# Kernel tuning notes

Measured on AMD Instinct MI355X. Metric: run time of the kernel, lower is better.

Reference implementation:

```python
import jax, jax.numpy as jnp
import numpy as np

HEAD = 8
D_Q = 64
NEG_INF = -1e9
EPS = 1e-9


def setup_inputs() -> dict:
    key = jax.random.key(0)
    ks = jax.random.split(key, 5)
    bs, seq_len, d_model = 4, 1024, 512
    context = jax.random.normal(ks[0], (bs, seq_len, d_model), dtype=jnp.float32)
    attention_mask = jnp.ones((bs, seq_len), dtype=jnp.int32)
    # nn.Linear default init: U(-1/sqrt(fan_in), 1/sqrt(fan_in))
    bound = 1.0 / np.sqrt(d_model)
    Wq = jax.random.uniform(ks[1], (HEAD * D_Q, d_model), jnp.float32, -bound, bound)
    bq = jax.random.uniform(ks[2], (HEAD * D_Q,), jnp.float32, -bound, bound)
    Wk = jax.random.uniform(ks[3], (HEAD * D_Q, d_model), jnp.float32, -bound, bound)
    bk = jax.random.uniform(ks[4], (HEAD * D_Q,), jnp.float32, -bound, bound)
    return {"context": context, "attention_mask": attention_mask,
            "Wq": Wq, "bq": bq, "Wk": Wk, "bk": bk}


def reference(context, attention_mask, Wq, bq, Wk, bk):
    bs, seq_len, d_model = context.shape
    # structural masks
    after_mask = jnp.eye(seq_len, k=1, dtype=jnp.int32)    # superdiagonal
    prev_mask = jnp.eye(seq_len, k=-1, dtype=jnp.int32)    # subdiagonal
    self_mask = jnp.eye(seq_len, dtype=jnp.int32)          # diagonal
    summing_op = jnp.triu(jnp.ones((seq_len, seq_len), jnp.float32))  # upper-tri ones

    # attention_mask & (after + prev): (bs,1,1,S) & (S,S) -> (bs,1,S,S)
    mask = attention_mask[:, None, None, :] & (after_mask + prev_mask)

    # projections -> (bs, head, seq, d_q)
    q = (context @ Wq.T + bq).reshape(bs, seq_len, HEAD, D_Q).transpose(0, 2, 1, 3)
    k = (context @ Wk.T + bk).reshape(bs, seq_len, HEAD, D_Q).transpose(0, 2, 1, 3)

    scores = jnp.einsum('bhqd,bhkd->bhqk', q, k) / d_model
    scores = jnp.where(mask == 0, NEG_INF, scores)
    scores = jax.nn.softmax(scores, axis=-1)

    # geometric-mean fusion of forward/backward neighbor scores
    phrasal_attn = jnp.sqrt(scores * jnp.swapaxes(scores, -2, -1) + EPS)
    # prior_attn = 0 (default): phrasal_attn = 0 + (1-0)*phrasal_attn

    # log-cumsum via triangular matmuls
    p = jnp.where(after_mask == 0, 0.0, jnp.log(phrasal_attn + EPS))  # (bs,h,S,S)
    p = jnp.einsum('bhij,jk->bhik', p, summing_op)
    attn = jnp.exp(jnp.einsum('ij,bhjk->bhik', summing_op, p))
    # zero out on-and-below diagonal (keep strict upper triangle)
    strict_upper = summing_op.astype(jnp.int32) - self_mask
    attn = jnp.where(strict_upper == 0, 0.0, attn)
    attn = attn + jnp.swapaxes(attn, -2, -1) + jnp.where(self_mask == 0, EPS, phrasal_attn)
    return (attn, phrasal_attn)
```

## Files before the change

kernel.cpp:

```cpp
#include <hip/hip_runtime.h>
#include <hip/hip_bf16.h>

#define BS 4
#define SEQ 1024
#define DM 512
#define NQK 1024
#define NROW (BS*SEQ)
#define EPS 1e-9f
#define SQRTEPS 3.16227766e-5f

typedef __attribute__((ext_vector_type(8))) short short8;
typedef __attribute__((ext_vector_type(4))) float floatx4;

__global__ __launch_bounds__(256) void convert_kernel(
    const float* __restrict__ ctx, const float* __restrict__ Wq,
    const float* __restrict__ Wk, unsigned short* __restrict__ Xbf,
    unsigned short* __restrict__ Wbf)
{
    int idx = blockIdx.x * 256 + threadIdx.x;
    {
        unsigned int u = __float_as_uint(ctx[idx]);
        Xbf[idx] = (unsigned short)((u + 0x7fffu + ((u >> 16) & 1u)) >> 16);
    }
    if (idx < DM * DM) {
        unsigned int a = __float_as_uint(Wq[idx]);
        Wbf[idx] = (unsigned short)((a + 0x7fffu + ((a >> 16) & 1u)) >> 16);
        unsigned int c = __float_as_uint(Wk[idx]);
        Wbf[DM * DM + idx] = (unsigned short)((c + 0x7fffu + ((c >> 16) & 1u)) >> 16);
    }
}

#define BM 64
#define BN 64
#define BK 32
#define LDA 40
#define NGEMM 1024
#define NBG   4096

__global__ __launch_bounds__(256) void gemm_qk_bg(
    const unsigned short* __restrict__ X, const unsigned short* __restrict__ W,
    const float* __restrict__ bq, const float* __restrict__ bk,
    float* __restrict__ QK, float* __restrict__ phrasal)
{
    __shared__ unsigned short As[BM * LDA];
    __shared__ unsigned short Bs[BN * LDA];

    const int id  = blockIdx.x;
    const int tid = threadIdx.x;

    if (id >= NGEMM) {
        const int bb = id - NGEMM;
        float* base = phrasal + (size_t)bb * 8192;
        floatx4 v4 = {SQRTEPS, SQRTEPS, SQRTEPS, SQRTEPS};
        #pragma unroll
        for (int j = 0; j < 8; ++j)
            *(floatx4*)(base + (size_t)(j * 256 + tid) * 4) = v4;
        return;
    }

    const int bm   = id & 63;
    const int bn   = id >> 6;
    const int wave = tid >> 6;
    const int lane = tid & 63;
    const int wm   = wave >> 1, wn = wave & 1;
    const int lr   = lane & 15;
    const int kg   = lane >> 4;

    const int srow = tid >> 2;
    const int skc  = (tid & 3) << 3;
    const unsigned short* Xp = X + (size_t)(bm * BM + srow) * DM + skc;
    const unsigned short* Wp = W + (size_t)(bn * BN + srow) * DM + skc;

    floatx4 acc[2][2] = {};

    for (int k0 = 0; k0 < DM; k0 += BK) {
        uint4 va = *(const uint4*)(Xp + k0);
        uint4 vb = *(const uint4*)(Wp + k0);
        __syncthreads();
        *(uint4*)(As + srow * LDA + skc) = va;
        *(uint4*)(Bs + srow * LDA + skc) = vb;
        __syncthreads();

        short8 a[2], b[2];
        #pragma unroll
        for (int mi = 0; mi < 2; ++mi)
            a[mi] = *(const short8*)(As + (wm * 32 + mi * 16 + lr) * LDA + kg * 8);
        #pragma unroll
        for (int ni = 0; ni < 2; ++ni)
            b[ni] = *(const short8*)(Bs + (wn * 32 + ni * 16 + lr) * LDA + kg * 8);
        #pragma unroll
        for (int mi = 0; mi < 2; ++mi)
            #pragma unroll
            for (int ni = 0; ni < 2; ++ni)
                acc[mi][ni] = __builtin_amdgcn_mfma_f32_16x16x32_bf16(
                    a[mi], b[ni], acc[mi][ni], 0, 0, 0);
    }

    #pragma unroll
    for (int mi = 0; mi < 2; ++mi) {
        #pragma unroll
        for (int ni = 0; ni < 2; ++ni) {
            int n = bn * BN + wn * 32 + ni * 16 + lr;
            float bias = (n < DM) ? bq[n] : bk[n - DM];
            #pragma unroll
            for (int r = 0; r < 4; ++r) {
                int m = bm * BM + wm * 32 + mi * 16 + kg * 4 + r;
                QK[(size_t)m * NQK + n] = acc[mi][ni][r] + bias;
            }
        }
    }
}

__global__ __launch_bounds__(256) void dot_kernel(
    const float* __restrict__ QK, float* __restrict__ uArr, float* __restrict__ vArr)
{
    const int gw   = blockIdx.x * 4 + (threadIdx.x >> 6);
    const int lane = threadIdx.x & 63;
    const int bh   = gw >> 10;
    const int i    = gw & 1023;
    const int b    = bh >> 3, h = bh & 7;

    float u = 0.f, v = 0.f;
    if (i < SEQ - 1) {
        const float* r0 = QK + (size_t)(b * SEQ + i)     * NQK;
        const float* r1 = QK + (size_t)(b * SEQ + i + 1) * NQK;
        float qi  = r0[h * 64 + lane];
        float ki  = r0[DM + h * 64 + lane];
        float qi1 = r1[h * 64 + lane];
        float ki1 = r1[DM + h * 64 + lane];
        float pu = qi * ki1, pv = qi1 * ki;
        #pragma unroll
        for (int m = 1; m < 64; m <<= 1) {
            pu += __shfl_xor(pu, m);
            pv += __shfl_xor(pv, m);
        }
        u = pu * (1.0f / DM);
        v = pv * (1.0f / DM);
    }
    if (lane == 0) { uArr[gw] = u; vArr[gw] = v; }
}

__global__ __launch_bounds__(1024) void gscan_kernel(
    const float* __restrict__ uArr, const float* __restrict__ vArr,
    const int* __restrict__ am, float* __restrict__ gArr, float* __restrict__ CArr)
{
    __shared__ double wsum[16];

    const int bh   = blockIdx.x;
    const int b    = bh >> 3;
    const int i    = threadIdx.x;
    const int base = bh * SEQ;

    float g = 0.f;
    if (i < SEQ - 1) {
        float u   = uArr[base + i];
        float vv  = vArr[base + i];
        int   im1 = (i > 0) ? i - 1 : 0;
        float vm1 = vArr[base + im1];
        float up1 = uArr[base + i + 1];
        int mL = (i > 0) ? am[b * SEQ + i - 1] : 0;
        int mR = am[b * SEQ + i + 1];
        float s_up = mR ? (mL ? 1.f / (1.f + expf(vm1 - u)) : 1.f) : 0.f;
        int mL2 = am[b * SEQ + i];
        int mR2 = (i + 2 < SEQ) ? am[b * SEQ + i + 2] : 0;
        float s_dn = mL2 ? (mR2 ? 1.f / (1.f + expf(up1 - vv)) : 1.f) : 0.f;
        g = sqrtf(s_up * s_dn + EPS);
        gArr[base + i] = g;
    }

    double L = (i < SEQ - 1) ? (double)logf(g + EPS) : 0.0;
    double x = L;
    const int lane = i & 63, wv = i >> 6;
    #pragma unroll
    for (int off = 1; off < 64; off <<= 1) {
        double t = __shfl_up(x, off);
        if (lane >= off) x += t;
    }
    if (lane == 63) wsum[wv] = x;
    __syncthreads();
    double pref = 0.0;
    for (int w = 0; w < wv; ++w) pref += wsum[w];
    CArr[base + i] = (float)(pref + x - L);
}

__global__ __launch_bounds__(256) void fill_attn(
    const float* __restrict__ gArr, const float* __restrict__ CArr,
    float* __restrict__ attn, float* __restrict__ phrasal)
{
    const int row = blockIdx.x;
    const int bh  = row >> 10;
    const int i   = row & 1023;
    const int t   = threadIdx.x;

    const float Ci = CArr[row];
    floatx4 c4 = *(const floatx4*)(CArr + bh * SEQ + t * 4);
    floatx4 av;
    #pragma unroll
    for (int j = 0; j < 4; ++j) {
        int k = t * 4 + j;
        float d = (k > i) ? (c4[j] - Ci) : (Ci - c4[j]);
        av[j] = (k == i) ? SQRTEPS : (__expf(d) + EPS);
    }
    *(floatx4*)(attn + (size_t)row * SEQ + t * 4) = av;

    if (t == 0) {
        if (i > 0)
            phrasal[(size_t)row * SEQ + i - 1] = gArr[bh * SEQ + i - 1];
        if (i < SEQ - 1)
            phrasal[(size_t)row * SEQ + i + 1] = gArr[bh * SEQ + i];
    }
}

extern "C" void kernel_launch(void* const* d_in, const int* in_sizes, int n_in,
                              void* d_out, int out_size, void* d_ws, size_t ws_size,
                              hipStream_t stream) {
    const float* ctx = (const float*)d_in[0];
    const int*   am  = (const int*)d_in[1];
    const float* Wq  = (const float*)d_in[2];
    const float* bq  = (const float*)d_in[3];
    const float* Wk  = (const float*)d_in[4];
    const float* bk  = (const float*)d_in[5];
    float* out = (float*)d_out;

    char* ws = (char*)d_ws;
    unsigned short* Xbf = (unsigned short*)(ws);
    unsigned short* Wbf = (unsigned short*)(ws + 4194304);
    float*          QK  = (float*)(ws + 5242880);
    float*          uA  = (float*)(ws + 22020096);
    float*          vA  = (float*)(ws + 22151168);
    float*          gA  = (float*)(ws + 22282240);
    float*          CA  = (float*)(ws + 22413312);

    float* attn_out    = out;
    float* phrasal_out = out + (size_t)BS * 8 * SEQ * SEQ;

    convert_kernel<<<dim3(BS * SEQ * DM / 256), 256, 0, stream>>>(ctx, Wq, Wk, Xbf, Wbf);
    gemm_qk_bg<<<dim3(NGEMM + NBG), 256, 0, stream>>>(Xbf, Wbf, bq, bk, QK, phrasal_out);
    dot_kernel<<<dim3(BS * 8 * SEQ / 4), 256, 0, stream>>>(QK, uA, vA);
    gscan_kernel<<<dim3(BS * 8), 1024, 0, stream>>>(uA, vA, am, gA, CA);
    fill_attn<<<dim3(BS * 8 * SEQ), 256, 0, stream>>>(gA, CA, attn_out, phrasal_out);
}
```

Baseline: 293.6 us.

## Spread phrasal background fill across gemm, dot and scan kernels; double GEMM K-tile

The constant background fill of the phrasal output is split across three launches: 2560 chunks ride with the GEMM, 1024 with the dot kernel and 512 with the scan kernel. Before, all of it was in the GEMM launch. Spreading the fill lets the memory-bound stores overlap with the GEMM, the latency-bound dot reductions and the tiny 32-block scan. Separately, the GEMM K tile grows from 32 to 64, halving the number of barrier-synchronised iterations at the cost of more shared memory per block.

```diff
diff --git a/kernel.cpp b/kernel.cpp
--- a/kernel.cpp
+++ b/kernel.cpp
@@ -12,6 +12,10 @@
 typedef __attribute__((ext_vector_type(8))) short short8;
 typedef __attribute__((ext_vector_type(4))) float floatx4;
 
+#define BG_GEMM 2560
+#define BG_DOT  1024
+#define BG_SCAN 512
+
 __global__ __launch_bounds__(256) void convert_kernel(
     const float* __restrict__ ctx, const float* __restrict__ Wq,
     const float* __restrict__ Wk, unsigned short* __restrict__ Xbf,
@@ -32,10 +36,9 @@
 
 #define BM 64
 #define BN 64
-#define BK 32
-#define LDA 40
+#define BK 64
+#define LDA 72
 #define NGEMM 1024
-#define NBG   4096
 
 __global__ __launch_bounds__(256) void gemm_qk_bg(
     const unsigned short* __restrict__ X, const unsigned short* __restrict__ W,
@@ -66,34 +69,41 @@
     const int lr   = lane & 15;
     const int kg   = lane >> 4;
 
-    const int srow = tid >> 2;
-    const int skc  = (tid & 3) << 3;
+    const int srow = tid >> 3;
+    const int skc  = (tid & 7) << 3;
     const unsigned short* Xp = X + (size_t)(bm * BM + srow) * DM + skc;
     const unsigned short* Wp = W + (size_t)(bn * BN + srow) * DM + skc;
 
     floatx4 acc[2][2] = {};
 
     for (int k0 = 0; k0 < DM; k0 += BK) {
-        uint4 va = *(const uint4*)(Xp + k0);
-        uint4 vb = *(const uint4*)(Wp + k0);
+        uint4 va0 = *(const uint4*)(Xp + k0);
+        uint4 va1 = *(const uint4*)(Xp + k0 + 32 * DM);
+        uint4 vb0 = *(const uint4*)(Wp + k0);
+        uint4 vb1 = *(const uint4*)(Wp + k0 + 32 * DM);
         __syncthreads();
-        *(uint4*)(As + srow * LDA + skc) = va;
-        *(uint4*)(Bs + srow * LDA + skc) = vb;
+        *(uint4*)(As + srow * LDA + skc)        = va0;
+        *(uint4*)(As + (srow + 32) * LDA + skc) = va1;
+        *(uint4*)(Bs + srow * LDA + skc)        = vb0;
+        *(uint4*)(Bs + (srow + 32) * LDA + skc) = vb1;
         __syncthreads();
 
-        short8 a[2], b[2];
-        #pragma unroll
-        for (int mi = 0; mi < 2; ++mi)
-            a[mi] = *(const short8*)(As + (wm * 32 + mi * 16 + lr) * LDA + kg * 8);
-        #pragma unroll
-        for (int ni = 0; ni < 2; ++ni)
-            b[ni] = *(const short8*)(Bs + (wn * 32 + ni * 16 + lr) * LDA + kg * 8);
-        #pragma unroll
-        for (int mi = 0; mi < 2; ++mi)
+        #pragma unroll
+        for (int ks = 0; ks < 2; ++ks) {
+            short8 a[2], b[2];
+            #pragma unroll
+            for (int mi = 0; mi < 2; ++mi)
+                a[mi] = *(const short8*)(As + (wm * 32 + mi * 16 + lr) * LDA + ks * 32 + kg * 8);
             #pragma unroll
             for (int ni = 0; ni < 2; ++ni)
-                acc[mi][ni] = __builtin_amdgcn_mfma_f32_16x16x32_bf16(
-                    a[mi], b[ni], acc[mi][ni], 0, 0, 0);
+                b[ni] = *(const short8*)(Bs + (wn * 32 + ni * 16 + lr) * LDA + ks * 32 + kg * 8);
+            #pragma unroll
+            for (int mi = 0; mi < 2; ++mi)
+                #pragma unroll
+                for (int ni = 0; ni < 2; ++ni)
+                    acc[mi][ni] = __builtin_amdgcn_mfma_f32_16x16x32_bf16(
+                        a[mi], b[ni], acc[mi][ni], 0, 0, 0);
+        }
     }
 
     #pragma unroll
@@ -111,10 +121,24 @@
     }
 }
 
+#define NDOT 8192
+
 __global__ __launch_bounds__(256) void dot_kernel(
-    const float* __restrict__ QK, float* __restrict__ uArr, float* __restrict__ vArr)
-{
-    const int gw   = blockIdx.x * 4 + (threadIdx.x >> 6);
+    const float* __restrict__ QK, float* __restrict__ uArr, float* __restrict__ vArr,
+    float* __restrict__ phrasal)
+{
+    const int id = blockIdx.x;
+    if (id >= NDOT) {
+        const int bb = id - NDOT;
+        float* base = phrasal + (size_t)(BG_GEMM + bb) * 8192;
+        floatx4 v4 = {SQRTEPS, SQRTEPS, SQRTEPS, SQRTEPS};
+        #pragma unroll
+        for (int j = 0; j < 8; ++j)
+            *(floatx4*)(base + (size_t)(j * 256 + threadIdx.x) * 4) = v4;
+        return;
+    }
+
+    const int gw   = id * 4 + (threadIdx.x >> 6);
     const int lane = threadIdx.x & 63;
     const int bh   = gw >> 10;
     const int i    = gw & 1023;
@@ -142,9 +166,20 @@
 
 __global__ __launch_bounds__(1024) void gscan_kernel(
     const float* __restrict__ uArr, const float* __restrict__ vArr,
-    const int* __restrict__ am, float* __restrict__ gArr, float* __restrict__ CArr)
+    const int* __restrict__ am, float* __restrict__ gArr, float* __restrict__ CArr,
+    float* __restrict__ phrasal)
 {
     __shared__ double wsum[16];
+
+    if (blockIdx.x >= 32) {
+        const int bb = blockIdx.x - 32;
+        float* base = phrasal + (size_t)(BG_GEMM + BG_DOT + bb) * 8192;
+        floatx4 v4 = {SQRTEPS, SQRTEPS, SQRTEPS, SQRTEPS};
+        #pragma unroll
+        for (int j = 0; j < 2; ++j)
+            *(floatx4*)(base + (size_t)(j * 1024 + threadIdx.x) * 4) = v4;
+        return;
+    }
 
     const int bh   = blockIdx.x;
     const int b    = bh >> 3;
@@ -235,8 +270,8 @@
     float* phrasal_out = out + (size_t)BS * 8 * SEQ * SEQ;
 
     convert_kernel<<<dim3(BS * SEQ * DM / 256), 256, 0, stream>>>(ctx, Wq, Wk, Xbf, Wbf);
-    gemm_qk_bg<<<dim3(NGEMM + NBG), 256, 0, stream>>>(Xbf, Wbf, bq, bk, QK, phrasal_out);
-    dot_kernel<<<dim3(BS * 8 * SEQ / 4), 256, 0, stream>>>(QK, uA, vA);
-    gscan_kernel<<<dim3(BS * 8), 1024, 0, stream>>>(uA, vA, am, gA, CA);
+    gemm_qk_bg<<<dim3(NGEMM + BG_GEMM), 256, 0, stream>>>(Xbf, Wbf, bq, bk, QK, phrasal_out);
+    dot_kernel<<<dim3(NDOT + BG_DOT), 256, 0, stream>>>(QK, uA, vA, phrasal_out);
+    gscan_kernel<<<dim3(32 + BG_SCAN), 1024, 0, stream>>>(uA, vA, am, gA, CA, phrasal_out);
     fill_attn<<<dim3(BS * 8 * SEQ), 256, 0, stream>>>(gA, CA, attn_out, phrasal_out);
 }
```

Measured after the change: 291.4 us. About the same (-0.7%).

## Fuse all stages into one persistent kernel with software grid barriers

Applied to the files above, without the earlier changes.

Merges the five launches (convert, GEMM, dot, scan, fill) into a single persistent kernel of 1024 blocks separated by atomic-counter grid barriers. The constant background writes of phrasal are spread across the blocks that sit idle in each phase. The GEMM is retiled to 128x64 with a K step of 64, and the fill stage writes 32 rows per block. This removes per-launch overhead and inter-kernel gaps. In exchange it relies on all 1024 blocks being co-resident for the barriers to avoid deadlock, and it adds spin-wait costs.

```diff
diff --git a/kernel.cpp b/kernel.cpp
--- a/kernel.cpp
+++ b/kernel.cpp
@@ -5,209 +5,243 @@
 #define SEQ 1024
 #define DM 512
 #define NQK 1024
-#define NROW (BS*SEQ)
 #define EPS 1e-9f
 #define SQRTEPS 3.16227766e-5f
+#define NBLK 1024
+#define LDA 72
 
 typedef __attribute__((ext_vector_type(8))) short short8;
 typedef __attribute__((ext_vector_type(4))) float floatx4;
 
-__global__ __launch_bounds__(256) void convert_kernel(
-    const float* __restrict__ ctx, const float* __restrict__ Wq,
-    const float* __restrict__ Wk, unsigned short* __restrict__ Xbf,
-    unsigned short* __restrict__ Wbf)
-{
-    int idx = blockIdx.x * 256 + threadIdx.x;
-    {
-        unsigned int u = __float_as_uint(ctx[idx]);
-        Xbf[idx] = (unsigned short)((u + 0x7fffu + ((u >> 16) & 1u)) >> 16);
-    }
-    if (idx < DM * DM) {
-        unsigned int a = __float_as_uint(Wq[idx]);
-        Wbf[idx] = (unsigned short)((a + 0x7fffu + ((a >> 16) & 1u)) >> 16);
-        unsigned int c = __float_as_uint(Wk[idx]);
-        Wbf[DM * DM + idx] = (unsigned short)((c + 0x7fffu + ((c >> 16) & 1u)) >> 16);
-    }
-}
-
-#define BM 64
-#define BN 64
-#define BK 32
-#define LDA 40
-#define NGEMM 1024
-#define NBG   4096
-
-__global__ __launch_bounds__(256) void gemm_qk_bg(
-    const unsigned short* __restrict__ X, const unsigned short* __restrict__ W,
-    const float* __restrict__ bq, const float* __restrict__ bk,
-    float* __restrict__ QK, float* __restrict__ phrasal)
-{
-    __shared__ unsigned short As[BM * LDA];
-    __shared__ unsigned short Bs[BN * LDA];
-
-    const int id  = blockIdx.x;
-    const int tid = threadIdx.x;
-
-    if (id >= NGEMM) {
-        const int bb = id - NGEMM;
-        float* base = phrasal + (size_t)bb * 8192;
-        floatx4 v4 = {SQRTEPS, SQRTEPS, SQRTEPS, SQRTEPS};
-        #pragma unroll
-        for (int j = 0; j < 8; ++j)
-            *(floatx4*)(base + (size_t)(j * 256 + tid) * 4) = v4;
-        return;
-    }
-
-    const int bm   = id & 63;
-    const int bn   = id >> 6;
-    const int wave = tid >> 6;
-    const int lane = tid & 63;
-    const int wm   = wave >> 1, wn = wave & 1;
-    const int lr   = lane & 15;
-    const int kg   = lane >> 4;
-
-    const int srow = tid >> 2;
-    const int skc  = (tid & 3) << 3;
-    const unsigned short* Xp = X + (size_t)(bm * BM + srow) * DM + skc;
-    const unsigned short* Wp = W + (size_t)(bn * BN + srow) * DM + skc;
-
-    floatx4 acc[2][2] = {};
-
-    for (int k0 = 0; k0 < DM; k0 += BK) {
-        uint4 va = *(const uint4*)(Xp + k0);
-        uint4 vb = *(const uint4*)(Wp + k0);
-        __syncthreads();
-        *(uint4*)(As + srow * LDA + skc) = va;
-        *(uint4*)(Bs + srow * LDA + skc) = vb;
-        __syncthreads();
-
-        short8 a[2], b[2];
-        #pragma unroll
-        for (int mi = 0; mi < 2; ++mi)
-            a[mi] = *(const short8*)(As + (wm * 32 + mi * 16 + lr) * LDA + kg * 8);
-        #pragma unroll
-        for (int ni = 0; ni < 2; ++ni)
-            b[ni] = *(const short8*)(Bs + (wn * 32 + ni * 16 + lr) * LDA + kg * 8);
-        #pragma unroll
-        for (int mi = 0; mi < 2; ++mi)
-            #pragma unroll
-            for (int ni = 0; ni < 2; ++ni)
-                acc[mi][ni] = __builtin_amdgcn_mfma_f32_16x16x32_bf16(
-                    a[mi], b[ni], acc[mi][ni], 0, 0, 0);
-    }
-
-    #pragma unroll
-    for (int mi = 0; mi < 2; ++mi) {
-        #pragma unroll
-        for (int ni = 0; ni < 2; ++ni) {
-            int n = bn * BN + wn * 32 + ni * 16 + lr;
-            float bias = (n < DM) ? bq[n] : bk[n - DM];
-            #pragma unroll
-            for (int r = 0; r < 4; ++r) {
-                int m = bm * BM + wm * 32 + mi * 16 + kg * 4 + r;
-                QK[(size_t)m * NQK + n] = acc[mi][ni][r] + bias;
-            }
-        }
-    }
-}
-
-__global__ __launch_bounds__(256) void dot_kernel(
-    const float* __restrict__ QK, float* __restrict__ uArr, float* __restrict__ vArr)
-{
-    const int gw   = blockIdx.x * 4 + (threadIdx.x >> 6);
-    const int lane = threadIdx.x & 63;
-    const int bh   = gw >> 10;
-    const int i    = gw & 1023;
-    const int b    = bh >> 3, h = bh & 7;
-
-    float u = 0.f, v = 0.f;
-    if (i < SEQ - 1) {
-        const float* r0 = QK + (size_t)(b * SEQ + i)     * NQK;
-        const float* r1 = QK + (size_t)(b * SEQ + i + 1) * NQK;
-        float qi  = r0[h * 64 + lane];
-        float ki  = r0[DM + h * 64 + lane];
-        float qi1 = r1[h * 64 + lane];
-        float ki1 = r1[DM + h * 64 + lane];
-        float pu = qi * ki1, pv = qi1 * ki;
-        #pragma unroll
-        for (int m = 1; m < 64; m <<= 1) {
-            pu += __shfl_xor(pu, m);
-            pv += __shfl_xor(pv, m);
-        }
-        u = pu * (1.0f / DM);
-        v = pv * (1.0f / DM);
-    }
-    if (lane == 0) { uArr[gw] = u; vArr[gw] = v; }
-}
-
-__global__ __launch_bounds__(1024) void gscan_kernel(
-    const float* __restrict__ uArr, const float* __restrict__ vArr,
-    const int* __restrict__ am, float* __restrict__ gArr, float* __restrict__ CArr)
-{
-    __shared__ double wsum[16];
-
-    const int bh   = blockIdx.x;
-    const int b    = bh >> 3;
-    const int i    = threadIdx.x;
-    const int base = bh * SEQ;
-
-    float g = 0.f;
-    if (i < SEQ - 1) {
-        float u   = uArr[base + i];
-        float vv  = vArr[base + i];
-        int   im1 = (i > 0) ? i - 1 : 0;
-        float vm1 = vArr[base + im1];
-        float up1 = uArr[base + i + 1];
-        int mL = (i > 0) ? am[b * SEQ + i - 1] : 0;
-        int mR = am[b * SEQ + i + 1];
-        float s_up = mR ? (mL ? 1.f / (1.f + expf(vm1 - u)) : 1.f) : 0.f;
-        int mL2 = am[b * SEQ + i];
-        int mR2 = (i + 2 < SEQ) ? am[b * SEQ + i + 2] : 0;
-        float s_dn = mL2 ? (mR2 ? 1.f / (1.f + expf(up1 - vv)) : 1.f) : 0.f;
-        g = sqrtf(s_up * s_dn + EPS);
-        gArr[base + i] = g;
-    }
-
-    double L = (i < SEQ - 1) ? (double)logf(g + EPS) : 0.0;
-    double x = L;
-    const int lane = i & 63, wv = i >> 6;
-    #pragma unroll
-    for (int off = 1; off < 64; off <<= 1) {
-        double t = __shfl_up(x, off);
-        if (lane >= off) x += t;
-    }
-    if (lane == 63) wsum[wv] = x;
+__device__ __forceinline__ unsigned short f2bf(float x) {
+    unsigned int u = __float_as_uint(x);
+    return (unsigned short)((u + 0x7fffu + ((u >> 16) & 1u)) >> 16);
+}
+
+__device__ __forceinline__ void gridbar(unsigned* cnt) {
     __syncthreads();
-    double pref = 0.0;
-    for (int w = 0; w < wv; ++w) pref += wsum[w];
-    CArr[base + i] = (float)(pref + x - L);
-}
-
-__global__ __launch_bounds__(256) void fill_attn(
-    const float* __restrict__ gArr, const float* __restrict__ CArr,
+    if (threadIdx.x == 0) {
+        __threadfence();
+        __hip_atomic_fetch_add(cnt, 1u, __ATOMIC_RELEASE, __HIP_MEMORY_SCOPE_AGENT);
+        while (__hip_atomic_load(cnt, __ATOMIC_ACQUIRE, __HIP_MEMORY_SCOPE_AGENT) < NBLK)
+            __builtin_amdgcn_s_sleep(2);
+        __threadfence();
+    }
+    __syncthreads();
+}
+
+__device__ __forceinline__ void bgwrite(float* base, int n_iters, int tid) {
+    floatx4 v4 = {SQRTEPS, SQRTEPS, SQRTEPS, SQRTEPS};
+    for (int j = 0; j < n_iters; ++j)
+        *(floatx4*)(base + (size_t)(j * 256 + tid) * 4) = v4;
+}
+
+__global__ __launch_bounds__(256, 4) void mega_kernel(
+    const float* __restrict__ ctx, const int* __restrict__ am,
+    const float* __restrict__ Wq, const float* __restrict__ bq,
+    const float* __restrict__ Wk, const float* __restrict__ bk,
+    unsigned short* __restrict__ Xbf, unsigned short* __restrict__ Wbf,
+    float* __restrict__ QK, float* __restrict__ uA, float* __restrict__ vA,
+    float* __restrict__ gA, float* __restrict__ CA, unsigned* __restrict__ cnt,
     float* __restrict__ attn, float* __restrict__ phrasal)
 {
-    const int row = blockIdx.x;
-    const int bh  = row >> 10;
-    const int i   = row & 1023;
-    const int t   = threadIdx.x;
-
-    const float Ci = CArr[row];
-    floatx4 c4 = *(const floatx4*)(CArr + bh * SEQ + t * 4);
-    floatx4 av;
-    #pragma unroll
-    for (int j = 0; j < 4; ++j) {
-        int k = t * 4 + j;
-        float d = (k > i) ? (c4[j] - Ci) : (Ci - c4[j]);
-        av[j] = (k == i) ? SQRTEPS : (__expf(d) + EPS);
-    }
-    *(floatx4*)(attn + (size_t)row * SEQ + t * 4) = av;
-
-    if (t == 0) {
-        if (i > 0)
-            phrasal[(size_t)row * SEQ + i - 1] = gArr[bh * SEQ + i - 1];
-        if (i < SEQ - 1)
-            phrasal[(size_t)row * SEQ + i + 1] = gArr[bh * SEQ + i];
+    __shared__ unsigned short As[128 * LDA];
+    __shared__ unsigned short Bs[64 * LDA];
+    __shared__ double wsum[4];
+
+    const int blk = blockIdx.x;
+    const int tid = threadIdx.x;
+
+    if (blk < 256) {
+        int gthr = blk * 256 + tid;
+        #pragma unroll
+        for (int j = 0; j < 40; ++j) {
+            int e = gthr + 65536 * j;
+            if (e < 2097152) {
+                Xbf[e] = f2bf(ctx[e]);
+            } else {
+                int e2 = e - 2097152;
+                float s = (e2 < 262144) ? Wq[e2] : Wk[e2 - 262144];
+                Wbf[e2] = f2bf(s);
+            }
+        }
+    } else {
+        bgwrite(phrasal + (size_t)(blk - 256) * 8192, 8, tid);
+    }
+    gridbar(cnt + 0);
+
+    if (blk < 512) {
+        const int bm = blk & 31, bn = blk >> 5;
+        const int wave = tid >> 6, lane = tid & 63;
+        const int lr = lane & 15, kg = lane >> 4;
+        const unsigned short* Xb = Xbf + (size_t)(bm * 128) * DM;
+        const unsigned short* Wb = Wbf + (size_t)(bn * 64) * DM;
+
+        floatx4 acc[2][4] = {};
+        for (int k0 = 0; k0 < DM; k0 += 64) {
+            uint4 va[4], vb[2];
+            #pragma unroll
+            for (int p = 0; p < 4; ++p) {
+                int c = tid + p * 256, row = c >> 3, kc = (c & 7) << 3;
+                va[p] = *(const uint4*)(Xb + (size_t)row * DM + k0 + kc);
+            }
+            #pragma unroll
+            for (int p = 0; p < 2; ++p) {
+                int c = tid + p * 256, row = c >> 3, kc = (c & 7) << 3;
+                vb[p] = *(const uint4*)(Wb + (size_t)row * DM + k0 + kc);
+            }
+            __syncthreads();
+            #pragma unroll
+            for (int p = 0; p < 4; ++p) {
+                int c = tid + p * 256, row = c >> 3, kc = (c & 7) << 3;
+                *(uint4*)(As + row * LDA + kc) = va[p];
+            }
+            #pragma unroll
+            for (int p = 0; p < 2; ++p) {
+                int c = tid + p * 256, row = c >> 3, kc = (c & 7) << 3;
+                *(uint4*)(Bs + row * LDA + kc) = vb[p];
+            }
+            __syncthreads();
+            #pragma unroll
+            for (int ks = 0; ks < 2; ++ks) {
+                short8 a[2], b[4];
+                #pragma unroll
+                for (int mi = 0; mi < 2; ++mi)
+                    a[mi] = *(const short8*)(As + (wave * 32 + mi * 16 + lr) * LDA + ks * 32 + kg * 8);
+                #pragma unroll
+                for (int ni = 0; ni < 4; ++ni)
+                    b[ni] = *(const short8*)(Bs + (ni * 16 + lr) * LDA + ks * 32 + kg * 8);
+                #pragma unroll
+                for (int mi = 0; mi < 2; ++mi)
+                    #pragma unroll
+                    for (int ni = 0; ni < 4; ++ni)
+                        acc[mi][ni] = __builtin_amdgcn_mfma_f32_16x16x32_bf16(
+                            a[mi], b[ni], acc[mi][ni], 0, 0, 0);
+            }
+        }
+        #pragma unroll
+        for (int mi = 0; mi < 2; ++mi) {
+            #pragma unroll
+            for (int ni = 0; ni < 4; ++ni) {
+                int n = bn * 64 + ni * 16 + lr;
+                float bias = (n < DM) ? bq[n] : bk[n - DM];
+                #pragma unroll
+                for (int r = 0; r < 4; ++r) {
+                    int m = bm * 128 + wave * 32 + mi * 16 + kg * 4 + r;
+                    QK[(size_t)m * NQK + n] = acc[mi][ni][r] + bias;
+                }
+            }
+        }
+    } else {
+        bgwrite(phrasal + 6291456 + (size_t)(blk - 512) * 32768, 32, tid);
+    }
+    gridbar(cnt + 1);
+
+    if (blk < 768) {
+        const int wv = tid >> 6, lane = tid & 63;
+        const int gwv = blk * 4 + wv;
+        for (int gw = gwv; gw < 32768; gw += 3072) {
+            int bh = gw >> 10, i = gw & 1023;
+            int b = bh >> 3, h = bh & 7;
+            float u = 0.f, v = 0.f;
+            if (i < SEQ - 1) {
+                const float* r0 = QK + (size_t)(b * SEQ + i) * NQK;
+                const float* r1 = r0 + NQK;
+                float qi  = r0[h * 64 + lane];
+                float ki  = r0[DM + h * 64 + lane];
+                float qi1 = r1[h * 64 + lane];
+                float ki1 = r1[DM + h * 64 + lane];
+                float pu = qi * ki1, pv = qi1 * ki;
+                #pragma unroll
+                for (int m = 1; m < 64; m <<= 1) {
+                    pu += __shfl_xor(pu, m);
+                    pv += __shfl_xor(pv, m);
+                }
+                u = pu * (1.0f / DM);
+                v = pv * (1.0f / DM);
+            }
+            if (lane == 0) { uA[gw] = u; vA[gw] = v; }
+        }
+    } else {
+        bgwrite(phrasal + 23068672 + (size_t)(blk - 768) * 24576, 24, tid);
+    }
+    gridbar(cnt + 2);
+
+    if (blk < 32) {
+        const int bh = blk, b = bh >> 3;
+        const int i0 = tid * 4;
+        floatx4 u4 = *(const floatx4*)(uA + bh * SEQ + i0);
+        floatx4 v4 = *(const floatx4*)(vA + bh * SEQ + i0);
+        float vm1f = (i0 > 0) ? vA[bh * SEQ + i0 - 1] : 0.f;
+        float up1l = (i0 + 4 < SEQ) ? uA[bh * SEQ + i0 + 4] : 0.f;
+        const int* amb = am + b * SEQ;
+
+        floatx4 g4;
+        double pref[4], tsum = 0.0;
+        #pragma unroll
+        for (int j = 0; j < 4; ++j) {
+            int i = i0 + j;
+            float g = 0.f;
+            if (i < SEQ - 1) {
+                float u = u4[j], vv = v4[j];
+                float vm1 = (j == 0) ? vm1f : v4[j - 1];
+                float up1 = (j == 3) ? up1l : u4[j + 1];
+                int mL = (i > 0) ? amb[i - 1] : 0;
+                int mR = amb[i + 1];
+                float s_up = mR ? (mL ? 1.f / (1.f + expf(vm1 - u)) : 1.f) : 0.f;
+                int mL2 = amb[i];
+                int mR2 = (i + 2 < SEQ) ? amb[i + 2] : 0;
+                float s_dn = mL2 ? (mR2 ? 1.f / (1.f + expf(up1 - vv)) : 1.f) : 0.f;
+                g = sqrtf(s_up * s_dn + EPS);
+            }
+            g4[j] = g;
+            float L = (i < SEQ - 1) ? logf(g + EPS) : 0.f;
+            pref[j] = tsum;
+            tsum += (double)L;
+        }
+        double x = tsum;
+        const int lane = tid & 63, wvv = tid >> 6;
+        #pragma unroll
+        for (int off = 1; off < 64; off <<= 1) {
+            double s = __shfl_up(x, off);
+            if (lane >= off) x += s;
+        }
+        if (lane == 63) wsum[wvv] = x;
+        __syncthreads();
+        double woff = 0.0;
+        for (int w = 0; w < wvv; ++w) woff += wsum[w];
+        double ex = woff + x - tsum;
+        floatx4 C4;
+        #pragma unroll
+        for (int j = 0; j < 4; ++j) C4[j] = (float)(ex + pref[j]);
+        *(floatx4*)(CA + bh * SEQ + i0) = C4;
+        *(floatx4*)(gA + bh * SEQ + i0) = g4;
+    } else if (blk < 544) {
+        bgwrite(phrasal + 29360128 + (size_t)(blk - 32) * 8192, 8, tid);
+    }
+    gridbar(cnt + 3);
+
+    {
+        const int bh = blk >> 5;
+        floatx4 c4 = *(const floatx4*)(CA + bh * SEQ + tid * 4);
+        const float* gb = gA + bh * SEQ;
+        for (int rr = 0; rr < 32; ++rr) {
+            int row = blk * 32 + rr;
+            int i = row & 1023;
+            float Ci = CA[row];
+            floatx4 av;
+            #pragma unroll
+            for (int j = 0; j < 4; ++j) {
+                int k = tid * 4 + j;
+                float d = (k > i) ? (c4[j] - Ci) : (Ci - c4[j]);
+                av[j] = (k == i) ? SQRTEPS : (__expf(d) + EPS);
+            }
+            *(floatx4*)(attn + (size_t)row * SEQ + tid * 4) = av;
+            if (tid == 0 && i > 0)
+                phrasal[(size_t)row * SEQ + i - 1] = gb[i - 1];
+            if (tid == 1 && i < SEQ - 1)
+                phrasal[(size_t)row * SEQ + i + 1] = gb[i];
+        }
     }
 }
 
@@ -230,13 +264,13 @@
     float*          vA  = (float*)(ws + 22151168);
     float*          gA  = (float*)(ws + 22282240);
     float*          CA  = (float*)(ws + 22413312);
+    unsigned*       cnt = (unsigned*)(ws + 22544384);
 
     float* attn_out    = out;
     float* phrasal_out = out + (size_t)BS * 8 * SEQ * SEQ;
 
-    convert_kernel<<<dim3(BS * SEQ * DM / 256), 256, 0, stream>>>(ctx, Wq, Wk, Xbf, Wbf);
-    gemm_qk_bg<<<dim3(NGEMM + NBG), 256, 0, stream>>>(Xbf, Wbf, bq, bk, QK, phrasal_out);
-    dot_kernel<<<dim3(BS * 8 * SEQ / 4), 256, 0, stream>>>(QK, uA, vA);
-    gscan_kernel<<<dim3(BS * 8), 1024, 0, stream>>>(uA, vA, am, gA, CA);
-    fill_attn<<<dim3(BS * 8 * SEQ), 256, 0, stream>>>(gA, CA, attn_out, phrasal_out);
-}
+    hipMemsetAsync(cnt, 0, 16, stream);
+    mega_kernel<<<dim3(NBLK), 256, 0, stream>>>(
+        ctx, am, Wq, bq, Wk, bk, Xbf, Wbf, QK, uA, vA, gA, CA, cnt,
+        attn_out, phrasal_out);
+}
```

Result: slower. 1.065 ms (+262.9%).

## Fuse QK projection with neighbor dot products and spread background fill across kernels

Applied to the files above, without the earlier changes.

The projection GEMM is retiled per (row-tile, head) so each block computes both Q and K for 64 rows and immediately forms the adjacent-row dot products in shared memory. This removes the full QK intermediate write and the separate dot kernel. Dot products that cross tile boundaries are patched in the scan kernel using saved first and last rows. The constant background fill of the phrasal output is split across the convert, gemm and scan kernels so it overlaps with compute, and the convert kernel is vectorized.

```diff
diff --git a/kernel.cpp b/kernel.cpp
--- a/kernel.cpp
+++ b/kernel.cpp
@@ -4,173 +4,220 @@
 #define BS 4
 #define SEQ 1024
 #define DM 512
-#define NQK 1024
-#define NROW (BS*SEQ)
 #define EPS 1e-9f
 #define SQRTEPS 3.16227766e-5f
 
 typedef __attribute__((ext_vector_type(8))) short short8;
 typedef __attribute__((ext_vector_type(4))) float floatx4;
+
+__device__ __forceinline__ unsigned short f2bf(float x) {
+    unsigned int u = __float_as_uint(x);
+    return (unsigned short)((u + 0x7fffu + ((u >> 16) & 1u)) >> 16);
+}
+
+__device__ __forceinline__ void bgwrite(float* base, int n_iters, int tid, int nthr) {
+    floatx4 v4 = {SQRTEPS, SQRTEPS, SQRTEPS, SQRTEPS};
+    for (int j = 0; j < n_iters; ++j)
+        *(floatx4*)(base + (size_t)(j * nthr + tid) * 4) = v4;
+}
 
 __global__ __launch_bounds__(256) void convert_kernel(
     const float* __restrict__ ctx, const float* __restrict__ Wq,
     const float* __restrict__ Wk, unsigned short* __restrict__ Xbf,
-    unsigned short* __restrict__ Wbf)
-{
-    int idx = blockIdx.x * 256 + threadIdx.x;
-    {
-        unsigned int u = __float_as_uint(ctx[idx]);
-        Xbf[idx] = (unsigned short)((u + 0x7fffu + ((u >> 16) & 1u)) >> 16);
-    }
-    if (idx < DM * DM) {
-        unsigned int a = __float_as_uint(Wq[idx]);
-        Wbf[idx] = (unsigned short)((a + 0x7fffu + ((a >> 16) & 1u)) >> 16);
-        unsigned int c = __float_as_uint(Wk[idx]);
-        Wbf[DM * DM + idx] = (unsigned short)((c + 0x7fffu + ((c >> 16) & 1u)) >> 16);
-    }
-}
-
-#define BM 64
-#define BN 64
-#define BK 32
-#define LDA 40
-#define NGEMM 1024
-#define NBG   4096
-
-__global__ __launch_bounds__(256) void gemm_qk_bg(
-    const unsigned short* __restrict__ X, const unsigned short* __restrict__ W,
+    unsigned short* __restrict__ Wbf, float* __restrict__ phrasal)
+{
+    const int blk = blockIdx.x, tid = threadIdx.x;
+    if (blk >= 256) {
+        bgwrite(phrasal + (size_t)(blk - 256) * 8192, 8, tid, 256);
+        return;
+    }
+    int gthr = blk * 256 + tid;
+    #pragma unroll
+    for (int j = 0; j < 10; ++j) {
+        int e4 = gthr + 65536 * j;
+        int e  = e4 * 4;
+        floatx4 s;
+        if (e < 2097152) {
+            s = *(const floatx4*)(ctx + e);
+        } else {
+            int e2 = e - 2097152;
+            s = (e2 < 262144) ? *(const floatx4*)(Wq + e2)
+                              : *(const floatx4*)(Wk + e2 - 262144);
+        }
+        ushort2 lo = {f2bf(s.x), f2bf(s.y)}, hi = {f2bf(s.z), f2bf(s.w)};
+        unsigned short* dst = (e < 2097152) ? (Xbf + e) : (Wbf + e - 2097152);
+        *(ushort2*)dst = lo;
+        *(ushort2*)(dst + 2) = hi;
+    }
+}
+
+#define NGEMM 512
+#define LDW 72
+#define LDQ 65
+
+__global__ __launch_bounds__(256) void gemmdot_kernel(
+    const unsigned short* __restrict__ Xbf, const unsigned short* __restrict__ Wbf,
     const float* __restrict__ bq, const float* __restrict__ bk,
-    float* __restrict__ QK, float* __restrict__ phrasal)
-{
-    __shared__ unsigned short As[BM * LDA];
-    __shared__ unsigned short Bs[BN * LDA];
-
-    const int id  = blockIdx.x;
-    const int tid = threadIdx.x;
-
-    if (id >= NGEMM) {
-        const int bb = id - NGEMM;
-        float* base = phrasal + (size_t)bb * 8192;
-        floatx4 v4 = {SQRTEPS, SQRTEPS, SQRTEPS, SQRTEPS};
-        #pragma unroll
-        for (int j = 0; j < 8; ++j)
-            *(floatx4*)(base + (size_t)(j * 256 + tid) * 4) = v4;
+    float* __restrict__ uA, float* __restrict__ vA,
+    float* __restrict__ qF, float* __restrict__ kF,
+    float* __restrict__ qL, float* __restrict__ kL,
+    float* __restrict__ phrasal)
+{
+    __shared__ char smem[2 * 64 * LDQ * 4];
+    unsigned short* Xs  = (unsigned short*)smem;
+    unsigned short* Wqs = Xs + 64 * LDW;
+    unsigned short* Wks = Wqs + 64 * LDW;
+    float* qS = (float*)smem;
+    float* kS = qS + 64 * LDQ;
+
+    const int blk = blockIdx.x, tid = threadIdx.x;
+    if (blk >= NGEMM) {
+        bgwrite(phrasal + (size_t)(768 + blk - NGEMM) * 8192, 8, tid, 256);
         return;
     }
 
-    const int bm   = id & 63;
-    const int bn   = id >> 6;
-    const int wave = tid >> 6;
-    const int lane = tid & 63;
-    const int wm   = wave >> 1, wn = wave & 1;
-    const int lr   = lane & 15;
-    const int kg   = lane >> 4;
-
-    const int srow = tid >> 2;
-    const int skc  = (tid & 3) << 3;
-    const unsigned short* Xp = X + (size_t)(bm * BM + srow) * DM + skc;
-    const unsigned short* Wp = W + (size_t)(bn * BN + srow) * DM + skc;
-
-    floatx4 acc[2][2] = {};
-
-    for (int k0 = 0; k0 < DM; k0 += BK) {
-        uint4 va = *(const uint4*)(Xp + k0);
-        uint4 vb = *(const uint4*)(Wp + k0);
+    const int rt = blk >> 3, h = blk & 7;
+    const int wv = tid >> 6, lane = tid & 63;
+    const int lr = lane & 15, kg = lane >> 4;
+
+    const int r0 = tid >> 3, kc0 = (tid & 7) << 3;
+    const unsigned short* Xb  = Xbf + (size_t)(rt * 64) * DM;
+    const unsigned short* Wqb = Wbf + (size_t)(h * 64) * DM;
+    const unsigned short* Wkb = Wbf + 262144 + (size_t)(h * 64) * DM;
+
+    floatx4 acc_q[4] = {}, acc_k[4] = {};
+
+    for (int k0 = 0; k0 < DM; k0 += 64) {
+        uint4 x0  = *(const uint4*)(Xb  + (size_t)r0 * DM + k0 + kc0);
+        uint4 x1  = *(const uint4*)(Xb  + (size_t)(r0 + 32) * DM + k0 + kc0);
+        uint4 wq0 = *(const uint4*)(Wqb + (size_t)r0 * DM + k0 + kc0);
+        uint4 wq1 = *(const uint4*)(Wqb + (size_t)(r0 + 32) * DM + k0 + kc0);
+        uint4 wk0 = *(const uint4*)(Wkb + (size_t)r0 * DM + k0 + kc0);
+        uint4 wk1 = *(const uint4*)(Wkb + (size_t)(r0 + 32) * DM + k0 + kc0);
         __syncthreads();
-        *(uint4*)(As + srow * LDA + skc) = va;
-        *(uint4*)(Bs + srow * LDA + skc) = vb;
+        *(uint4*)(Xs  + r0 * LDW + kc0)        = x0;
+        *(uint4*)(Xs  + (r0 + 32) * LDW + kc0) = x1;
+        *(uint4*)(Wqs + r0 * LDW + kc0)        = wq0;
+        *(uint4*)(Wqs + (r0 + 32) * LDW + kc0) = wq1;
+        *(uint4*)(Wks + r0 * LDW + kc0)        = wk0;
+        *(uint4*)(Wks + (r0 + 32) * LDW + kc0) = wk1;
         __syncthreads();
-
-        short8 a[2], b[2];
-        #pragma unroll
-        for (int mi = 0; mi < 2; ++mi)
-            a[mi] = *(const short8*)(As + (wm * 32 + mi * 16 + lr) * LDA + kg * 8);
-        #pragma unroll
-        for (int ni = 0; ni < 2; ++ni)
-            b[ni] = *(const short8*)(Bs + (wn * 32 + ni * 16 + lr) * LDA + kg * 8);
-        #pragma unroll
-        for (int mi = 0; mi < 2; ++mi)
+        #pragma unroll
+        for (int ks = 0; ks < 2; ++ks) {
+            short8 a = *(const short8*)(Xs + (wv * 16 + lr) * LDW + ks * 32 + kg * 8);
             #pragma unroll
-            for (int ni = 0; ni < 2; ++ni)
-                acc[mi][ni] = __builtin_amdgcn_mfma_f32_16x16x32_bf16(
-                    a[mi], b[ni], acc[mi][ni], 0, 0, 0);
-    }
-
-    #pragma unroll
-    for (int mi = 0; mi < 2; ++mi) {
-        #pragma unroll
-        for (int ni = 0; ni < 2; ++ni) {
-            int n = bn * BN + wn * 32 + ni * 16 + lr;
-            float bias = (n < DM) ? bq[n] : bk[n - DM];
-            #pragma unroll
-            for (int r = 0; r < 4; ++r) {
-                int m = bm * BM + wm * 32 + mi * 16 + kg * 4 + r;
-                QK[(size_t)m * NQK + n] = acc[mi][ni][r] + bias;
+            for (int ni = 0; ni < 4; ++ni) {
+                short8 bqf = *(const short8*)(Wqs + (ni * 16 + lr) * LDW + ks * 32 + kg * 8);
+                acc_q[ni] = __builtin_amdgcn_mfma_f32_16x16x32_bf16(a, bqf, acc_q[ni], 0, 0, 0);
+                short8 bkf = *(const short8*)(Wks + (ni * 16 + lr) * LDW + ks * 32 + kg * 8);
+                acc_k[ni] = __builtin_amdgcn_mfma_f32_16x16x32_bf16(a, bkf, acc_k[ni], 0, 0, 0);
             }
         }
     }
-}
-
-__global__ __launch_bounds__(256) void dot_kernel(
-    const float* __restrict__ QK, float* __restrict__ uArr, float* __restrict__ vArr)
-{
-    const int gw   = blockIdx.x * 4 + (threadIdx.x >> 6);
-    const int lane = threadIdx.x & 63;
-    const int bh   = gw >> 10;
-    const int i    = gw & 1023;
-    const int b    = bh >> 3, h = bh & 7;
-
-    float u = 0.f, v = 0.f;
-    if (i < SEQ - 1) {
-        const float* r0 = QK + (size_t)(b * SEQ + i)     * NQK;
-        const float* r1 = QK + (size_t)(b * SEQ + i + 1) * NQK;
-        float qi  = r0[h * 64 + lane];
-        float ki  = r0[DM + h * 64 + lane];
-        float qi1 = r1[h * 64 + lane];
-        float ki1 = r1[DM + h * 64 + lane];
-        float pu = qi * ki1, pv = qi1 * ki;
+
+    __syncthreads();
+    #pragma unroll
+    for (int ni = 0; ni < 4; ++ni) {
+        float bqv = bq[h * 64 + ni * 16 + lr];
+        float bkv = bk[h * 64 + ni * 16 + lr];
+        #pragma unroll
+        for (int r = 0; r < 4; ++r) {
+            int row = wv * 16 + kg * 4 + r;
+            qS[row * LDQ + ni * 16 + lr] = acc_q[ni][r] + bqv;
+            kS[row * LDQ + ni * 16 + lr] = acc_k[ni][r] + bkv;
+        }
+    }
+    __syncthreads();
+
+    const int eb = (rt * 8 + h) * 64;
+    if (tid < 64) {
+        qF[eb + tid] = qS[tid];
+        kF[eb + tid] = kS[tid];
+    } else if (tid >= 192) {
+        int l = tid - 192;
+        qL[eb + l] = qS[63 * LDQ + l];
+        kL[eb + l] = kS[63 * LDQ + l];
+    }
+
+    for (int p = wv; p < 63; p += 4) {
+        float pu = qS[p * LDQ + lane] * kS[(p + 1) * LDQ + lane];
+        float pv = qS[(p + 1) * LDQ + lane] * kS[p * LDQ + lane];
         #pragma unroll
         for (int m = 1; m < 64; m <<= 1) {
             pu += __shfl_xor(pu, m);
             pv += __shfl_xor(pv, m);
         }
-        u = pu * (1.0f / DM);
-        v = pv * (1.0f / DM);
-    }
-    if (lane == 0) { uArr[gw] = u; vArr[gw] = v; }
+        if (lane == 0) {
+            int r = rt * 64 + p;
+            int idx = (((r >> 10) * 8 + h) << 10) | (r & 1023);
+            uA[idx] = pu * (1.0f / DM);
+            vA[idx] = pv * (1.0f / DM);
+        }
+    }
 }
 
 __global__ __launch_bounds__(1024) void gscan_kernel(
-    const float* __restrict__ uArr, const float* __restrict__ vArr,
-    const int* __restrict__ am, float* __restrict__ gArr, float* __restrict__ CArr)
-{
+    const float* __restrict__ uA, const float* __restrict__ vA,
+    const float* __restrict__ qF, const float* __restrict__ kF,
+    const float* __restrict__ qL, const float* __restrict__ kL,
+    const int* __restrict__ am, float* __restrict__ gA, float* __restrict__ CA,
+    float* __restrict__ phrasal)
+{
+    __shared__ float uS[SEQ], vS[SEQ];
+    __shared__ float uFix[16], vFix[16];
     __shared__ double wsum[16];
 
-    const int bh   = blockIdx.x;
-    const int b    = bh >> 3;
-    const int i    = threadIdx.x;
+    const int blk = blockIdx.x, i = threadIdx.x;
+    if (blk >= 32) {
+        bgwrite(phrasal + (size_t)(2816 + blk - 32) * 8192, 2, i, 1024);
+        return;
+    }
+
+    const int bh = blk, b = bh >> 3, h = bh & 7;
     const int base = bh * SEQ;
+    const int wv = i >> 6, lane = i & 63;
+
+    uS[i] = uA[base + i];
+    vS[i] = vA[base + i];
+
+    if (wv < 15) {
+        int e0 = ((b * 16 + wv) * 8 + h) * 64;
+        int e1 = e0 + 8 * 64;
+        float pu = qL[e0 + lane] * kF[e1 + lane];
+        float pv = qF[e1 + lane] * kL[e0 + lane];
+        #pragma unroll
+        for (int m = 1; m < 64; m <<= 1) {
+            pu += __shfl_xor(pu, m);
+            pv += __shfl_xor(pv, m);
+        }
+        if (lane == 0) { uFix[wv] = pu * (1.0f / DM); vFix[wv] = pv * (1.0f / DM); }
+    }
+    __syncthreads();
+    if ((i & 63) == 63) {
+        int j = i >> 6;
+        uS[i] = (j < 15) ? uFix[j] : 0.f;
+        vS[i] = (j < 15) ? vFix[j] : 0.f;
+    }
+    __syncthreads();
 
     float g = 0.f;
     if (i < SEQ - 1) {
-        float u   = uArr[base + i];
-        float vv  = vArr[base + i];
-        int   im1 = (i > 0) ? i - 1 : 0;
-        float vm1 = vArr[base + im1];
-        float up1 = uArr[base + i + 1];
-        int mL = (i > 0) ? am[b * SEQ + i - 1] : 0;
-        int mR = am[b * SEQ + i + 1];
+        float u = uS[i], vv = vS[i];
+        float vm1 = (i > 0) ? vS[i - 1] : 0.f;
+        float up1 = uS[i + 1];
+        const int* amb = am + b * SEQ;
+        int mL = (i > 0) ? amb[i - 1] : 0;
+        int mR = amb[i + 1];
         float s_up = mR ? (mL ? 1.f / (1.f + expf(vm1 - u)) : 1.f) : 0.f;
-        int mL2 = am[b * SEQ + i];
-        int mR2 = (i + 2 < SEQ) ? am[b * SEQ + i + 2] : 0;
+        int mL2 = amb[i];
+        int mR2 = (i + 2 < SEQ) ? amb[i + 2] : 0;
         float s_dn = mL2 ? (mR2 ? 1.f / (1.f + expf(up1 - vv)) : 1.f) : 0.f;
         g = sqrtf(s_up * s_dn + EPS);
-        gArr[base + i] = g;
+        gA[base + i] = g;
     }
 
     double L = (i < SEQ - 1) ? (double)logf(g + EPS) : 0.0;
     double x = L;
-    const int lane = i & 63, wv = i >> 6;
     #pragma unroll
     for (int off = 1; off < 64; off <<= 1) {
         double t = __shfl_up(x, off);
@@ -180,11 +227,11 @@
     __syncthreads();
     double pref = 0.0;
     for (int w = 0; w < wv; ++w) pref += wsum[w];
-    CArr[base + i] = (float)(pref + x - L);
+    CA[base + i] = (float)(pref + x - L);
 }
 
 __global__ __launch_bounds__(256) void fill_attn(
-    const float* __restrict__ gArr, const float* __restrict__ CArr,
+    const float* __restrict__ gA, const float* __restrict__ CA,
     float* __restrict__ attn, float* __restrict__ phrasal)
 {
     const int row = blockIdx.x;
@@ -192,8 +239,8 @@
     const int i   = row & 1023;
     const int t   = threadIdx.x;
 
-    const float Ci = CArr[row];
-    floatx4 c4 = *(const floatx4*)(CArr + bh * SEQ + t * 4);
+    const float Ci = CA[row];
+    floatx4 c4 = *(const floatx4*)(CA + bh * SEQ + t * 4);
     floatx4 av;
     #pragma unroll
     for (int j = 0; j < 4; ++j) {
@@ -203,12 +250,10 @@
     }
     *(floatx4*)(attn + (size_t)row * SEQ + t * 4) = av;
 
-    if (t == 0) {
-        if (i > 0)
-            phrasal[(size_t)row * SEQ + i - 1] = gArr[bh * SEQ + i - 1];
-        if (i < SEQ - 1)
-            phrasal[(size_t)row * SEQ + i + 1] = gArr[bh * SEQ + i];
-    }
+    if (t == 0 && i > 0)
+        phrasal[(size_t)row * SEQ + i - 1] = gA[bh * SEQ + i - 1];
+    if (t == 1 && i < SEQ - 1)
+        phrasal[(size_t)row * SEQ + i + 1] = gA[bh * SEQ + i];
 }
 
 extern "C" void kernel_launch(void* const* d_in, const int* in_sizes, int n_in,
@@ -225,18 +270,22 @@
     char* ws = (char*)d_ws;
     unsigned short* Xbf = (unsigned short*)(ws);
     unsigned short* Wbf = (unsigned short*)(ws + 4194304);
-    float*          QK  = (float*)(ws + 5242880);
-    float*          uA  = (float*)(ws + 22020096);
-    float*          vA  = (float*)(ws + 22151168);
-    float*          gA  = (float*)(ws + 22282240);
-    float*          CA  = (float*)(ws + 22413312);
+    float*          uA  = (float*)(ws + 5242880);
+    float*          vA  = (float*)(ws + 5373952);
+    float*          gA  = (float*)(ws + 5505024);
+    float*          CA  = (float*)(ws + 5636096);
+    float*          qF  = (float*)(ws + 5767168);
+    float*          kF  = (float*)(ws + 5898240);
+    float*          qL  = (float*)(ws + 6029312);
+    float*          kL  = (float*)(ws + 6160384);
 
     float* attn_out    = out;
     float* phrasal_out = out + (size_t)BS * 8 * SEQ * SEQ;
 
-    convert_kernel<<<dim3(BS * SEQ * DM / 256), 256, 0, stream>>>(ctx, Wq, Wk, Xbf, Wbf);
-    gemm_qk_bg<<<dim3(NGEMM + NBG), 256, 0, stream>>>(Xbf, Wbf, bq, bk, QK, phrasal_out);
-    dot_kernel<<<dim3(BS * 8 * SEQ / 4), 256, 0, stream>>>(QK, uA, vA);
-    gscan_kernel<<<dim3(BS * 8), 1024, 0, stream>>>(uA, vA, am, gA, CA);
+    convert_kernel<<<dim3(256 + 768), 256, 0, stream>>>(ctx, Wq, Wk, Xbf, Wbf, phrasal_out);
+    gemmdot_kernel<<<dim3(NGEMM + 2048), 256, 0, stream>>>(
+        Xbf, Wbf, bq, bk, uA, vA, qF, kF, qL, kL, phrasal_out);
+    gscan_kernel<<<dim3(32 + 1280), 1024, 0, stream>>>(
+        uA, vA, qF, kF, qL, kL, am, gA, CA, phrasal_out);
     fill_attn<<<dim3(BS * 8 * SEQ), 256, 0, stream>>>(gA, CA, attn_out, phrasal_out);
 }
```

Measured after the change: 290.7 us (median of 2 runs). About the same (-1.0%).
